# Kernel optimization log

Hardware: AMD Instinct MI355X
Metric: run time of the kernel (lower is better)

## Reference

```python
import jax, jax.numpy as jnp
import numpy as np

SELF_INTERACTION = True
TRIL_OFFSET = 0 if SELF_INTERACTION else -1


def setup_inputs() -> dict:
    key = jax.random.key(0)
    k1, k2 = jax.random.split(key)
    B, D, S = 16384, 128, 26
    dense_feature = jax.random.normal(k1, (B, D), dtype=jnp.float32)
    sparse_stack = jax.random.normal(k2, (S, B, D), dtype=jnp.float32)
    return {"dense_feature": dense_feature, "sparse_stack": sparse_stack}


def reference(dense_feature, sparse_stack):
    # dense_feature: [B, D]; sparse_stack: [S, B, D] (packed list of sparse features)
    B, D = dense_feature.shape
    # cat = torch.cat([dense] + sparse, dim=1).view(B, N, D)  -> feature-major order
    cat = jnp.concatenate([dense_feature[None], sparse_stack], axis=0)  # [N, B, D]
    cat = jnp.transpose(cat, (1, 0, 2))  # [B, N, D]
    N = cat.shape[1]
    # pairwise dot products: [B, N, N]
    interaction = jnp.einsum("bnd,bmd->bnm", cat, cat)
    i, j = np.tril_indices(N, k=TRIL_OFFSET)  # static indices
    tri = interaction[:, i, j]  # [B, N*(N+1)/2] (or N*(N-1)/2)
    return jnp.concatenate([dense_feature, tri], axis=1)
```

## Files before the change

### kernel.cpp

```cpp
#include <hip/hip_runtime.h>

#define B_TOTAL 16384
#define D 128
#define NROWS 27
#define BT 16
#define DC 32
#define NCHUNK (D / DC)
#define NSTRIDE 524
#define LDSROWS 30
#define OSTRIDE 386
#define OUTC 506

__global__ __launch_bounds__(256, 2)
void dotint_kernel(const float* __restrict__ dense,
                   const float* __restrict__ sparse,
                   float* __restrict__ out)
{
    __shared__ float lds[LDSROWS * NSTRIDE];

    const int tid = threadIdx.x;
    const int b0  = blockIdx.x * BT;
    const int e   = tid >> 4;
    const int s   = tid & 15;

    const int sc = (s < 15) ? s : 14;
    const int gi = (sc >= 1) + (sc >= 3) + (sc >= 6) + (sc >= 10);
    const int gj = sc - ((gi * (gi + 1)) >> 1);
    const int i0 = 6 * gi;
    const int j0 = 6 * gj;

    const int lane = tid & 63;
    const int wave = tid >> 6;
    const int sq   = lane & 7;
    const int seh  = lane >> 3;

    const int eswz = e & 7;

    float acc[6][6];
    #pragma unroll
    for (int a = 0; a < 6; ++a)
        #pragma unroll
        for (int b = 0; b < 6; ++b) acc[a][b] = 0.f;

    #pragma unroll 1
    for (int c = 0; c < NCHUNK; ++c) {
        const int dc0 = c * DC;
        for (int r2 = wave; r2 < NROWS * 2; r2 += 4) {
            const int n = r2 >> 1;
            const int h = r2 & 1;
            const int el = h * 8 + seh;
            const float* srcbase = (n == 0)
                ? dense
                : sparse + (size_t)(n - 1) * (size_t)B_TOTAL * D;
            const float* src = srcbase + (size_t)(b0 + el) * D + dc0
                             + (size_t)((sq ^ (el & 7)) * 4);
            __builtin_amdgcn_global_load_lds(
                (const __attribute__((address_space(1))) void*)src,
                (__attribute__((address_space(3))) void*)&lds[n * NSTRIDE + h * 256],
                16, 0, 0);
        }
        __syncthreads();

        #pragma unroll
        for (int q = 0; q < 8; ++q) {
            const int slot = (q ^ eswz) * 4;
            float4 ri[6], rj[6];
            #pragma unroll
            for (int k = 0; k < 6; ++k)
                ri[k] = *reinterpret_cast<const float4*>(
                    &lds[(i0 + k) * NSTRIDE + e * 32 + slot]);
            #pragma unroll
            for (int k = 0; k < 6; ++k)
                rj[k] = *reinterpret_cast<const float4*>(
                    &lds[(j0 + k) * NSTRIDE + e * 32 + slot]);
            #pragma unroll
            for (int a = 0; a < 6; ++a)
                #pragma unroll
                for (int b = 0; b < 6; ++b) {
                    acc[a][b] = fmaf(ri[a].x, rj[b].x, acc[a][b]);
                    acc[a][b] = fmaf(ri[a].y, rj[b].y, acc[a][b]);
                    acc[a][b] = fmaf(ri[a].z, rj[b].z, acc[a][b]);
                    acc[a][b] = fmaf(ri[a].w, rj[b].w, acc[a][b]);
                }
        }
        __syncthreads();
    }

    if (s < 15) {
        #pragma unroll
        for (int a = 0; a < 6; ++a) {
            const int i = i0 + a;
            if (i < NROWS) {
                const int ibase = (i * (i + 1)) >> 1;
                #pragma unroll
                for (int b = 0; b < 6; ++b) {
                    const int j = j0 + b;
                    if (j < NROWS && j <= i)
                        lds[e * OSTRIDE + ibase + j] = acc[a][b];
                }
            }
        }
    }
    __syncthreads();

    float* oblk = out + (size_t)b0 * OUTC;
    #pragma unroll
    for (int k = 0; k < 16; ++k) {
        const int f2 = tid + k * 256;
        if (f2 < 8 * OUTC) {
            const int b = f2 / 253;
            const int cc = 2 * f2 - b * OUTC;
            float2 v;
            if (cc < D) {
                v = *reinterpret_cast<const float2*>(dense + (size_t)(b0 + b) * D + cc);
            } else {
                v = *reinterpret_cast<const float2*>(&lds[b * OSTRIDE + (cc - D)]);
            }
            *reinterpret_cast<float2*>(oblk + (size_t)b * OUTC + cc) = v;
        }
    }
}

extern "C" void kernel_launch(void* const* d_in, const int* in_sizes, int n_in,
                              void* d_out, int out_size, void* d_ws, size_t ws_size,
                              hipStream_t stream)
{
    const float* dense  = (const float*)d_in[0];
    const float* sparse = (const float*)d_in[1];
    float* out          = (float*)d_out;

    dim3 grid(B_TOTAL / BT);
    dim3 block(256);
    hipLaunchKernelGGL(dotint_kernel, grid, block, 0, stream, dense, sparse, out);
}
```

Before: 337.0 us.

## Register-prefetch next feature chunk to overlap global loads with LDS compute

Replaces direct global-to-LDS loads with a register prefetch of 14 float4s per thread: the next chunk is loaded into registers while the current chunk is computed from LDS, then written to LDS between barriers. Row indices are clamped to 26 so the LDS array can shrink from 30 to 27 rows. The aim is to hide global memory latency behind the FMA loop. The cost is 56 extra VGPRs per thread under launch_bounds(256,2), which may cause spills or reduce occupancy.

Result: slower. 450.6 us (+33.7%).

```diff
diff --git a/kernel.cpp b/kernel.cpp
--- a/kernel.cpp
+++ b/kernel.cpp
@@ -7,16 +7,17 @@
 #define DC 32
 #define NCHUNK (D / DC)
 #define NSTRIDE 524
-#define LDSROWS 30
 #define OSTRIDE 386
 #define OUTC 506
+#define NF4 (NROWS * BT * (DC / 4))
+#define PF_MAX 14
 
 __global__ __launch_bounds__(256, 2)
 void dotint_kernel(const float* __restrict__ dense,
                    const float* __restrict__ sparse,
                    float* __restrict__ out)
 {
-    __shared__ float lds[LDSROWS * NSTRIDE];
+    __shared__ float lds[NROWS * NSTRIDE];
 
     const int tid = threadIdx.x;
     const int b0  = blockIdx.x * BT;
@@ -28,13 +29,48 @@
     const int gj = sc - ((gi * (gi + 1)) >> 1);
     const int i0 = 6 * gi;
     const int j0 = 6 * gj;
+    const int eswz = e & 7;
 
-    const int lane = tid & 63;
-    const int wave = tid >> 6;
-    const int sq   = lane & 7;
-    const int seh  = lane >> 3;
+    int rib[6], rjb[6];
+    #pragma unroll
+    for (int k = 0; k < 6; ++k) {
+        int ri_ = i0 + k; if (ri_ > 26) ri_ = 26;
+        int rj_ = j0 + k; if (rj_ > 26) rj_ = 26;
+        rib[k] = ri_ * NSTRIDE + e * 32;
+        rjb[k] = rj_ * NSTRIDE + e * 32;
+    }
 
-    const int eswz = e & 7;
+    float4 pf[PF_MAX];
+
+    auto load_chunk = [&](int c) {
+        #pragma unroll
+        for (int k = 0; k < PF_MAX; ++k) {
+            const int f = tid + k * 256;
+            if (f < NF4) {
+                const int n  = f >> 7;
+                const int el = (f >> 3) & 15;
+                const int g  = f & 7;
+                const float* base = (n == 0)
+                    ? dense
+                    : sparse + (size_t)(n - 1) * ((size_t)B_TOTAL * D);
+                pf[k] = *reinterpret_cast<const float4*>(
+                    base + (size_t)(b0 + el) * D + c * DC + g * 4);
+            }
+        }
+    };
+    auto write_chunk = [&]() {
+        #pragma unroll
+        for (int k = 0; k < PF_MAX; ++k) {
+            const int f = tid + k * 256;
+            if (f < NF4) {
+                const int n  = f >> 7;
+                const int el = (f >> 3) & 15;
+                const int g  = f & 7;
+                *reinterpret_cast<float4*>(
+                    &lds[n * NSTRIDE + el * 32 + ((g ^ (el & 7)) << 2)]) = pf[k];
+            }
+        }
+    };
 
     float acc[6][6];
     #pragma unroll
@@ -42,37 +78,25 @@
         #pragma unroll
         for (int b = 0; b < 6; ++b) acc[a][b] = 0.f;
 
+    load_chunk(0);
+
     #pragma unroll 1
     for (int c = 0; c < NCHUNK; ++c) {
-        const int dc0 = c * DC;
-        for (int r2 = wave; r2 < NROWS * 2; r2 += 4) {
-            const int n = r2 >> 1;
-            const int h = r2 & 1;
-            const int el = h * 8 + seh;
-            const float* srcbase = (n == 0)
-                ? dense
-                : sparse + (size_t)(n - 1) * (size_t)B_TOTAL * D;
-            const float* src = srcbase + (size_t)(b0 + el) * D + dc0
-                             + (size_t)((sq ^ (el & 7)) * 4);
-            __builtin_amdgcn_global_load_lds(
-                (const __attribute__((address_space(1))) void*)src,
-                (__attribute__((address_space(3))) void*)&lds[n * NSTRIDE + h * 256],
-                16, 0, 0);
-        }
         __syncthreads();
+        write_chunk();
+        __syncthreads();
+        if (c < NCHUNK - 1) load_chunk(c + 1);
 
         #pragma unroll
         for (int q = 0; q < 8; ++q) {
-            const int slot = (q ^ eswz) * 4;
+            const int s4 = (q ^ eswz) << 2;
             float4 ri[6], rj[6];
             #pragma unroll
             for (int k = 0; k < 6; ++k)
-                ri[k] = *reinterpret_cast<const float4*>(
-                    &lds[(i0 + k) * NSTRIDE + e * 32 + slot]);
+                ri[k] = *reinterpret_cast<const float4*>(&lds[rib[k] + s4]);
             #pragma unroll
             for (int k = 0; k < 6; ++k)
-                rj[k] = *reinterpret_cast<const float4*>(
-                    &lds[(j0 + k) * NSTRIDE + e * 32 + slot]);
+                rj[k] = *reinterpret_cast<const float4*>(&lds[rjb[k] + s4]);
             #pragma unroll
             for (int a = 0; a < 6; ++a)
                 #pragma unroll
@@ -83,9 +107,9 @@
                     acc[a][b] = fmaf(ri[a].w, rj[b].w, acc[a][b]);
                 }
         }
-        __syncthreads();
     }
 
+    __syncthreads();
     if (s < 15) {
         #pragma unroll
         for (int a = 0; a < 6; ++a) {
```

## Double-buffer LDS staging with smaller 8-row blocks and prefetch next chunk

Applied to the files above, without the earlier changes.

Shrinks each block to 8 batch rows and 128 threads and splits LDS into two buffers. The next D-chunk is prefetched with global_load_lds while the current one is computed, using a partial vmcnt wait and raw barriers in place of the two full syncthreads per chunk. Row base offsets are precomputed and clamped so the padded LDS rows are no longer needed. This is meant to hide global load latency behind the FMA work, at the cost of more blocks and fragile hand-tuned waitcnt and barrier ordering.

Result: slower. 347.2 us (+3.0%).

```diff
diff --git a/kernel.cpp b/kernel.cpp
--- a/kernel.cpp
+++ b/kernel.cpp
@@ -3,20 +3,20 @@
 #define B_TOTAL 16384
 #define D 128
 #define NROWS 27
-#define BT 16
+#define BT 8
 #define DC 32
 #define NCHUNK (D / DC)
-#define NSTRIDE 524
-#define LDSROWS 30
+#define RS 260
+#define BUFSZ (NROWS * RS)
 #define OSTRIDE 386
 #define OUTC 506
 
-__global__ __launch_bounds__(256, 2)
+__global__ __launch_bounds__(128, 1)
 void dotint_kernel(const float* __restrict__ dense,
                    const float* __restrict__ sparse,
                    float* __restrict__ out)
 {
-    __shared__ float lds[LDSROWS * NSTRIDE];
+    __shared__ float lds[2 * BUFSZ];
 
     const int tid = threadIdx.x;
     const int b0  = blockIdx.x * BT;
@@ -29,12 +29,32 @@
     const int i0 = 6 * gi;
     const int j0 = 6 * gj;
 
+    int rib[6], rjb[6];
+    #pragma unroll
+    for (int k = 0; k < 6; ++k) {
+        int ri_ = i0 + k; if (ri_ > 26) ri_ = 26;
+        int rj_ = j0 + k; if (rj_ > 26) rj_ = 26;
+        rib[k] = ri_ * RS + e * 32;
+        rjb[k] = rj_ * RS + e * 32;
+    }
+
+    const int wave = tid >> 6;
     const int lane = tid & 63;
-    const int wave = tid >> 6;
+    const int el   = lane >> 3;
     const int sq   = lane & 7;
-    const int seh  = lane >> 3;
 
-    const int eswz = e & 7;
+    auto stage = [&](int c, int buf) {
+        for (int n = wave; n < NROWS; n += 2) {
+            const float* base = (n == 0)
+                ? dense
+                : sparse + (size_t)(n - 1) * ((size_t)B_TOTAL * D);
+            const float* src = base + (size_t)(b0 + el) * D + c * DC + ((sq ^ el) << 2);
+            __builtin_amdgcn_global_load_lds(
+                (const __attribute__((address_space(1))) void*)src,
+                (__attribute__((address_space(3))) void*)&lds[buf * BUFSZ + n * RS],
+                16, 0, 0);
+        }
+    };
 
     float acc[6][6];
     #pragma unroll
@@ -42,37 +62,36 @@
         #pragma unroll
         for (int b = 0; b < 6; ++b) acc[a][b] = 0.f;
 
+    stage(0, 0);
+
     #pragma unroll 1
     for (int c = 0; c < NCHUNK; ++c) {
-        const int dc0 = c * DC;
-        for (int r2 = wave; r2 < NROWS * 2; r2 += 4) {
-            const int n = r2 >> 1;
-            const int h = r2 & 1;
-            const int el = h * 8 + seh;
-            const float* srcbase = (n == 0)
-                ? dense
-                : sparse + (size_t)(n - 1) * (size_t)B_TOTAL * D;
-            const float* src = srcbase + (size_t)(b0 + el) * D + dc0
-                             + (size_t)((sq ^ (el & 7)) * 4);
-            __builtin_amdgcn_global_load_lds(
-                (const __attribute__((address_space(1))) void*)src,
-                (__attribute__((address_space(3))) void*)&lds[n * NSTRIDE + h * 256],
-                16, 0, 0);
+        if (c > 0) {
+            asm volatile("" ::: "memory");
+            __builtin_amdgcn_s_barrier();
+            asm volatile("" ::: "memory");
         }
-        __syncthreads();
+        if (c + 1 < NCHUNK) {
+            stage(c + 1, (c + 1) & 1);
+            asm volatile("s_waitcnt vmcnt(13)" ::: "memory");
+        } else {
+            asm volatile("s_waitcnt vmcnt(0)" ::: "memory");
+        }
+        __builtin_amdgcn_sched_barrier(0);
+        __builtin_amdgcn_s_barrier();
+        asm volatile("" ::: "memory");
 
+        const float* bp = &lds[(c & 1) * BUFSZ];
         #pragma unroll
         for (int q = 0; q < 8; ++q) {
-            const int slot = (q ^ eswz) * 4;
+            const int s4 = (q ^ e) << 2;
             float4 ri[6], rj[6];
             #pragma unroll
             for (int k = 0; k < 6; ++k)
-                ri[k] = *reinterpret_cast<const float4*>(
-                    &lds[(i0 + k) * NSTRIDE + e * 32 + slot]);
+                ri[k] = *reinterpret_cast<const float4*>(&bp[rib[k] + s4]);
             #pragma unroll
             for (int k = 0; k < 6; ++k)
-                rj[k] = *reinterpret_cast<const float4*>(
-                    &lds[(j0 + k) * NSTRIDE + e * 32 + slot]);
+                rj[k] = *reinterpret_cast<const float4*>(&bp[rjb[k] + s4]);
             #pragma unroll
             for (int a = 0; a < 6; ++a)
                 #pragma unroll
@@ -83,9 +102,9 @@
                     acc[a][b] = fmaf(ri[a].w, rj[b].w, acc[a][b]);
                 }
         }
-        __syncthreads();
     }
 
+    __syncthreads();
     if (s < 15) {
         #pragma unroll
         for (int a = 0; a < 6; ++a) {
@@ -106,8 +125,8 @@
     float* oblk = out + (size_t)b0 * OUTC;
     #pragma unroll
     for (int k = 0; k < 16; ++k) {
-        const int f2 = tid + k * 256;
-        if (f2 < 8 * OUTC) {
+        const int f2 = tid + k * 128;
+        if (f2 < 4 * OUTC) {
             const int b = f2 / 253;
             const int cc = 2 * f2 - b * OUTC;
             float2 v;
@@ -130,6 +149,6 @@
     float* out          = (float*)d_out;
 
     dim3 grid(B_TOTAL / BT);
-    dim3 block(256);
+    dim3 block(128);
     hipLaunchKernelGGL(dotint_kernel, grid, block, 0, stream, dense, sparse, out);
 }
```
